# Kernel tuning notes

Measured on AMD Instinct MI355X. Metric: run time of the kernel, lower is better.

## Reference

```python
import jax, jax.numpy as jnp
import numpy as np

B, T, NG, NP, DV = 256, 100, 4096, 512, 2


def setup_inputs() -> dict:
    key = jax.random.key(0)
    k = jax.random.split(key, 6)
    v = jax.random.normal(k[0], (B, T, DV), dtype=jnp.float32) * 0.1
    P0 = jax.random.uniform(k[1], (B, NP), dtype=jnp.float32)
    # Dense kernels (glorot-ish scale); recurrent kernel uniform(-0.02, 0.02) per the module
    W_enc = jax.random.normal(k[2], (NP, NG), dtype=jnp.float32) / np.sqrt(NP)
    W_in = jax.random.normal(k[3], (DV, NG), dtype=jnp.float32) / np.sqrt(DV)
    W_rec = (jax.random.uniform(k[4], (NG, NG), dtype=jnp.float32) * 2.0 - 1.0) * 0.02
    W_dec = jax.random.normal(k[5], (NG, NP), dtype=jnp.float32) / np.sqrt(NG)
    return {"v": v, "P0": P0, "W_enc": W_enc, "W_in": W_in, "W_rec": W_rec, "W_dec": W_dec}


def reference(v, P0, W_enc, W_in, W_rec, W_dec):
    # encoder: init hidden state from place-cell code P0  -> [B, Ng]
    h0 = P0 @ W_enc
    # Precompute input projection for all timesteps: [B, T, Ng] -> scan over T
    xW = jnp.einsum('btd,dg->btg', v, W_in)
    xW_t = jnp.swapaxes(xW, 0, 1)  # [T, B, Ng]

    def step(h, x):
        h_new = jax.nn.relu(x + h @ W_rec)
        return h_new, h_new

    _, g = jax.lax.scan(step, h0, xW_t)      # g: [T, B, Ng]
    g = jnp.swapaxes(g, 0, 1)                # [B, T, Ng]
    place_preds = jnp.einsum('btg,gp->btp', g, W_dec)  # [B, T, Np]
    return place_preds
```

## Files before the change

kernel.cpp:

```cpp
#include <hip/hip_runtime.h>
#include <hip/hip_bf16.h>

typedef __attribute__((ext_vector_type(8))) short bf16x8;
typedef __attribute__((ext_vector_type(4))) float f32x4;

#define MFMA __builtin_amdgcn_mfma_f32_16x16x32_bf16

__device__ __forceinline__ short f2bf(float f) {
    union { __hip_bfloat16 h; short s; } u;
    u.h = __float2bfloat16(f);
    return u.s;
}

__global__ __launch_bounds__(64) void cvt_tile(const float* __restrict__ in,
                                               __hip_bfloat16* __restrict__ out, int C) {
    const int cd32 = C >> 5;
    const int tile = blockIdx.x;
    const int r16 = tile / cd32, c32 = tile - r16 * cd32;
    const int l = threadIdx.x;
    const int row = (r16 << 4) + (l & 15);
    const int c0 = (c32 << 5) + ((l >> 4) << 3);
    const float* src = in + (size_t)row * C + c0;
    short o[8];
#pragma unroll
    for (int j = 0; j < 8; ++j) o[j] = f2bf(src[j]);
    *(bf16x8*)((char*)out + (size_t)tile * 1024 + (l << 4)) = *(bf16x8*)o;
}

__global__ __launch_bounds__(256) void tcvt256(const float* __restrict__ in,
                                               __hip_bfloat16* __restrict__ out,
                                               int N, int K) {
    __shared__ float tile[64][65];
    const int r0 = blockIdx.x << 6;
    const int c0 = blockIdx.y << 6;
    const int tid = threadIdx.x;
    const int row = tid >> 2, cq = tid & 3;
#pragma unroll
    for (int it = 0; it < 4; ++it) {
        int c4 = cq + (it << 2);
        float4 vv = *(const float4*)(in + (size_t)(r0 + row) * N + c0 + (c4 << 2));
        tile[row][(c4 << 2) + 0] = vv.x;
        tile[row][(c4 << 2) + 1] = vv.y;
        tile[row][(c4 << 2) + 2] = vv.z;
        tile[row][(c4 << 2) + 3] = vv.w;
    }
    __syncthreads();
    const int kd32 = K >> 5;
#pragma unroll
    for (int half = 0; half < 2; ++half) {
        int slot = tid + (half << 8);
        int ti = slot >> 6, l = slot & 63;
        int ci = ti & 3, ri = ti >> 2;
        short o[8];
#pragma unroll
        for (int j = 0; j < 8; ++j)
            o[j] = f2bf(tile[(ri << 5) + ((l >> 4) << 3) + j][(ci << 4) + (l & 15)]);
        size_t tidx = (size_t)((c0 >> 4) + ci) * kd32 + (r0 >> 5) + ri;
        *(bf16x8*)((char*)out + tidx * 1024 + (l << 4)) = *(bf16x8*)o;
    }
}

template <int MODE, int NW, int KC>
__global__ __launch_bounds__(NW * 64) void gemm_r(const __hip_bfloat16* __restrict__ A,
                                                  const __hip_bfloat16* __restrict__ B,
                                                  void* __restrict__ outp,
                                                  const float* __restrict__ v,
                                                  const float* __restrict__ Wi, int t) {
    constexpr int KD32 = KC * NW;
    __shared__ __align__(16) char lds[NW * 16384];
    const int id = blockIdx.x;
    int bm, bn;
    if constexpr (MODE == 2) {
        int xcd = id & 7, idx = id >> 3;
        int sw = xcd * 400 + idx;
        bm = sw >> 3;
        bn = sw & 7;
    } else {
        int xcd = id & 7, j = id >> 3;
        bn = (xcd << 3) + (j & 7);
        bm = j >> 3;
    }
    const int tid = threadIdx.x, wv = tid >> 6, lane = tid & 63;
    char* myl = lds + (wv << 14);
    const int kw0 = wv * KC;
    const int bm4 = bm << 2, bn4 = bn << 2;

    constexpr size_t FSTR = (size_t)KD32 << 10;
    const char* pA = (const char*)A + (((size_t)(bm4 * KD32 + kw0)) << 10) + (lane << 4);
    const char* pB = (const char*)B + (((size_t)(bn4 * KD32 + kw0)) << 10) + (lane << 4);

    f32x4 acc[4][4] = {};
    bf16x8 A00, A01, A02, A03, A10, A11, A12, A13,
           A20, A21, A22, A23, A30, A31, A32, A33;
    bf16x8 B00, B01, B02, B03, B10, B11, B12, B13,
           B20, B21, B22, B23, B30, B31, B32, B33;

#define LOADG(S, KI)                                       \
    do {                                                   \
        const char* pa_ = pA + ((size_t)(KI) << 10);       \
        const char* pb_ = pB + ((size_t)(KI) << 10);       \
        A##S##0 = *(const bf16x8*)(pa_);                   \
        A##S##1 = *(const bf16x8*)(pa_ + FSTR);            \
        A##S##2 = *(const bf16x8*)(pa_ + 2 * FSTR);        \
        A##S##3 = *(const bf16x8*)(pa_ + 3 * FSTR);        \
        B##S##0 = *(const bf16x8*)(pb_);                   \
        B##S##1 = *(const bf16x8*)(pb_ + FSTR);            \
        B##S##2 = *(const bf16x8*)(pb_ + 2 * FSTR);        \
        B##S##3 = *(const bf16x8*)(pb_ + 3 * FSTR);        \
    } while (0)

#define COMPUTE(S)                                             \
    do {                                                       \
        acc[0][0] = MFMA(A##S##0, B##S##0, acc[0][0], 0, 0, 0);\
        acc[0][1] = MFMA(A##S##0, B##S##1, acc[0][1], 0, 0, 0);\
        acc[0][2] = MFMA(A##S##0, B##S##2, acc[0][2], 0, 0, 0);\
        acc[0][3] = MFMA(A##S##0, B##S##3, acc[0][3], 0, 0, 0);\
        acc[1][0] = MFMA(A##S##1, B##S##0, acc[1][0], 0, 0, 0);\
        acc[1][1] = MFMA(A##S##1, B##S##1, acc[1][1], 0, 0, 0);\
        acc[1][2] = MFMA(A##S##1, B##S##2, acc[1][2], 0, 0, 0);\
        acc[1][3] = MFMA(A##S##1, B##S##3, acc[1][3], 0, 0, 0);\
        acc[2][0] = MFMA(A##S##2, B##S##0, acc[2][0], 0, 0, 0);\
        acc[2][1] = MFMA(A##S##2, B##S##1, acc[2][1], 0, 0, 0);\
        acc[2][2] = MFMA(A##S##2, B##S##2, acc[2][2], 0, 0, 0);\
        acc[2][3] = MFMA(A##S##2, B##S##3, acc[2][3], 0, 0, 0);\
        acc[3][0] = MFMA(A##S##3, B##S##0, acc[3][0], 0, 0, 0);\
        acc[3][1] = MFMA(A##S##3, B##S##1, acc[3][1], 0, 0, 0);\
        acc[3][2] = MFMA(A##S##3, B##S##2, acc[3][2], 0, 0, 0);\
        acc[3][3] = MFMA(A##S##3, B##S##3, acc[3][3], 0, 0, 0);\
    } while (0)

#define ITER(S, SP, DOISS, KI)                  \
    do {                                        \
        if (DOISS) LOADG(SP, (KI) + 3);         \
        __builtin_amdgcn_sched_barrier(0);      \
        COMPUTE(S);                             \
        __builtin_amdgcn_sched_barrier(0);      \
    } while (0)

    LOADG(0, 0);
    __builtin_amdgcn_sched_barrier(0);
    LOADG(1, 1);
    __builtin_amdgcn_sched_barrier(0);
    LOADG(2, 2);
    __builtin_amdgcn_sched_barrier(0);

    int s = 0;
    for (; s + 4 < KC; s += 4) {
        ITER(0, 3, true, s + 0);
        ITER(1, 0, true, s + 1);
        ITER(2, 1, true, s + 2);
        ITER(3, 2, true, s + 3);
    }
    ITER(0, 3, true,  s + 0);
    ITER(1, 0, false, s + 1);
    ITER(2, 1, false, s + 2);
    ITER(3, 2, false, s + 3);

#undef ITER
#undef COMPUTE
#undef LOADG

#pragma unroll
    for (int f = 0; f < 4; ++f)
#pragma unroll
        for (int g = 0; g < 4; ++g)
            *(f32x4*)(myl + (((f << 2) + g) << 10) + (lane << 4)) = acc[f][g];
    __syncthreads();

    constexpr int FPW = 16 / NW;
    f32x4 fin[FPW];
#pragma unroll
    for (int q = 0; q < FPW; ++q) {
        const int fid = wv * FPW + q;
        f32x4 ssum = {};
#pragma unroll
        for (int w = 0; w < NW; ++w)
            ssum += *(const f32x4*)(lds + (w << 14) + (fid << 10) + (lane << 4));
        fin[q] = ssum;
    }

    if constexpr (MODE == 0 || MODE == 1) {
        char* O = (char*)outp;
#pragma unroll
        for (int q = 0; q < FPW; ++q) {
            const int fid = wv * FPW + q;
            const int fr = fid >> 2, g = fid & 3;
            const int rbase = (bm << 6) + (fr << 4) + ((lane >> 4) << 2);
            const int c = (bn << 6) + (g << 4) + (lane & 15);
#pragma unroll
            for (int j = 0; j < 4; ++j) {
                int r = rbase + j;
                float val = fin[q][j];
                if constexpr (MODE == 1) {
                    float v0 = v[(size_t)(r * 100 + t) * 2 + 0];
                    float v1 = v[(size_t)(r * 100 + t) * 2 + 1];
                    val = fmaxf(val + v0 * Wi[c] + v1 * Wi[4096 + c], 0.0f);
                }
                size_t off = ((size_t)(r >> 4) * 128 + (c >> 5)) * 1024 +
                             ((size_t)((r & 15) + (((c >> 3) & 3) << 4)) << 4) +
                             ((c & 7) << 1);
                *(short*)(O + off) = f2bf(val);
            }
        }
    } else {
        float* O = (float*)outp;
#pragma unroll
        for (int q = 0; q < FPW; ++q) {
            const int fid = wv * FPW + q;
            const int fr = fid >> 2, g = fid & 3;
            const int rbase = (bm << 6) + (fr << 4) + ((lane >> 4) << 2);
            const int c = (bn << 6) + (g << 4) + (lane & 15);
#pragma unroll
            for (int j = 0; j < 4; ++j) {
                int r = rbase + j;
                int tt = r >> 8;
                int b = r & 255;
                O[((size_t)b * 100 + tt) * 512 + c] = fin[q][j];
            }
        }
    }
}

extern "C" void kernel_launch(void* const* d_in, const int* in_sizes, int n_in,
                              void* d_out, int out_size, void* d_ws, size_t ws_size,
                              hipStream_t stream) {
    const float* v     = (const float*)d_in[0];
    const float* P0    = (const float*)d_in[1];
    const float* W_enc = (const float*)d_in[2];
    const float* W_in  = (const float*)d_in[3];
    const float* W_rec = (const float*)d_in[4];
    const float* W_dec = (const float*)d_in[5];
    float* out = (float*)d_out;

    char* ws = (char*)d_ws;
    __hip_bfloat16* Wrt = (__hip_bfloat16*)(ws + 0);
    __hip_bfloat16* Wet = (__hip_bfloat16*)(ws + 33554432);
    __hip_bfloat16* Wdt = (__hip_bfloat16*)(ws + 37748736);
    __hip_bfloat16* P0t = (__hip_bfloat16*)(ws + 41943040);
    __hip_bfloat16* h0  = (__hip_bfloat16*)(ws + 42205184);
    __hip_bfloat16* G   = (__hip_bfloat16*)(ws + 44302336);

    tcvt256<<<dim3(64, 64), 256, 0, stream>>>(W_rec, Wrt, 4096, 4096);
    tcvt256<<<dim3(8, 64), 256, 0, stream>>>(W_enc, Wet, 4096, 512);
    tcvt256<<<dim3(64, 8), 256, 0, stream>>>(W_dec, Wdt, 512, 4096);
    cvt_tile<<<256, 64, 0, stream>>>(P0, P0t, 512);

    gemm_r<0, 4, 4><<<256, 256, 0, stream>>>(P0t, Wet, (void*)h0, nullptr, nullptr, 0);

    for (int t = 0; t < 100; ++t) {
        const __hip_bfloat16* hprev = (t == 0) ? h0 : (G + (size_t)(t - 1) * 1048576);
        gemm_r<1, 4, 32><<<256, 256, 0, stream>>>(hprev, Wrt,
                                                  (void*)(G + (size_t)t * 1048576), v, W_in, t);
    }

    gemm_r<2, 4, 32><<<3200, 256, 0, stream>>>(G, Wdt, (void*)out, nullptr, nullptr, 0);
}
```

Measured before the change: 1.511 ms.

## Replace split-K decoder GEMM with dedicated 128x128 tiled kernel

The final decoder projection (25600x4096 by 4096x512) moves off the generic split-K gemm_r path, which used 64x64 tiles, 4 waves reducing over K through LDS, and 3200 blocks. It now uses a new gemm_d kernel with 128x128 output tiles, where each of the 4 waves owns a 64x64 sub-tile over the full K. This removes the LDS reduction and raises operand reuse per load, at the cost of longer per-wave K loops and only 800 blocks.

```diff
diff --git a/kernel.cpp b/kernel.cpp
--- a/kernel.cpp
+++ b/kernel.cpp
@@ -69,17 +69,9 @@
     constexpr int KD32 = KC * NW;
     __shared__ __align__(16) char lds[NW * 16384];
     const int id = blockIdx.x;
-    int bm, bn;
-    if constexpr (MODE == 2) {
-        int xcd = id & 7, idx = id >> 3;
-        int sw = xcd * 400 + idx;
-        bm = sw >> 3;
-        bn = sw & 7;
-    } else {
-        int xcd = id & 7, j = id >> 3;
-        bn = (xcd << 3) + (j & 7);
-        bm = j >> 3;
-    }
+    const int xcd = id & 7, j = id >> 3;
+    const int bn = (xcd << 3) + (j & 7);
+    const int bm = j >> 3;
     const int tid = threadIdx.x, wv = tid >> 6, lane = tid & 63;
     char* myl = lds + (wv << 14);
     const int kw0 = wv * KC;
@@ -179,43 +171,132 @@
         fin[q] = ssum;
     }
 
-    if constexpr (MODE == 0 || MODE == 1) {
-        char* O = (char*)outp;
-#pragma unroll
-        for (int q = 0; q < FPW; ++q) {
-            const int fid = wv * FPW + q;
-            const int fr = fid >> 2, g = fid & 3;
-            const int rbase = (bm << 6) + (fr << 4) + ((lane >> 4) << 2);
-            const int c = (bn << 6) + (g << 4) + (lane & 15);
-#pragma unroll
-            for (int j = 0; j < 4; ++j) {
-                int r = rbase + j;
-                float val = fin[q][j];
-                if constexpr (MODE == 1) {
-                    float v0 = v[(size_t)(r * 100 + t) * 2 + 0];
-                    float v1 = v[(size_t)(r * 100 + t) * 2 + 1];
-                    val = fmaxf(val + v0 * Wi[c] + v1 * Wi[4096 + c], 0.0f);
-                }
-                size_t off = ((size_t)(r >> 4) * 128 + (c >> 5)) * 1024 +
-                             ((size_t)((r & 15) + (((c >> 3) & 3) << 4)) << 4) +
-                             ((c & 7) << 1);
-                *(short*)(O + off) = f2bf(val);
+    char* O = (char*)outp;
+#pragma unroll
+    for (int q = 0; q < FPW; ++q) {
+        const int fid = wv * FPW + q;
+        const int fr = fid >> 2, g = fid & 3;
+        const int rbase = (bm << 6) + (fr << 4) + ((lane >> 4) << 2);
+        const int c = (bn << 6) + (g << 4) + (lane & 15);
+#pragma unroll
+        for (int j = 0; j < 4; ++j) {
+            int r = rbase + j;
+            float val = fin[q][j];
+            if constexpr (MODE == 1) {
+                float v0 = v[(size_t)(r * 100 + t) * 2 + 0];
+                float v1 = v[(size_t)(r * 100 + t) * 2 + 1];
+                val = fmaxf(val + v0 * Wi[c] + v1 * Wi[4096 + c], 0.0f);
             }
+            size_t off = ((size_t)(r >> 4) * 128 + (c >> 5)) * 1024 +
+                         ((size_t)((r & 15) + (((c >> 3) & 3) << 4)) << 4) +
+                         ((c & 7) << 1);
+            *(short*)(O + off) = f2bf(val);
         }
-    } else {
-        float* O = (float*)outp;
-#pragma unroll
-        for (int q = 0; q < FPW; ++q) {
-            const int fid = wv * FPW + q;
-            const int fr = fid >> 2, g = fid & 3;
-            const int rbase = (bm << 6) + (fr << 4) + ((lane >> 4) << 2);
-            const int c = (bn << 6) + (g << 4) + (lane & 15);
+    }
+}
+
+__global__ __launch_bounds__(256) void gemm_d(const __hip_bfloat16* __restrict__ G,
+                                              const __hip_bfloat16* __restrict__ Wdt,
+                                              float* __restrict__ out) {
+    constexpr int KD32 = 128;
+    const int id = blockIdx.x;
+    const int xcd = id & 7, idx = id >> 3;
+    const int sw = xcd * 100 + idx;
+    const int bm = sw >> 2;
+    const int bn = sw & 3;
+    const int tid = threadIdx.x, wv = tid >> 6, lane = tid & 63;
+    const int wr = wv >> 1, wc = wv & 1;
+
+    const int slab = bm >> 1, half = bm & 1;
+    constexpr size_t FSTR = (size_t)KD32 << 10;
+    const char* pA = (const char*)G + (size_t)slab * 2097152 +
+                     ((size_t)((half << 3) + (wr << 2)) << 17) + (lane << 4);
+    const char* pB = (const char*)Wdt +
+                     ((size_t)((bn << 3) + (wc << 2)) << 17) + (lane << 4);
+
+    f32x4 acc[4][4] = {};
+    bf16x8 A00, A01, A02, A03, A10, A11, A12, A13,
+           A20, A21, A22, A23, A30, A31, A32, A33;
+    bf16x8 B00, B01, B02, B03, B10, B11, B12, B13,
+           B20, B21, B22, B23, B30, B31, B32, B33;
+
+#define LOADG(S, KI)                                       \
+    do {                                                   \
+        const char* pa_ = pA + ((size_t)(KI) << 10);       \
+        const char* pb_ = pB + ((size_t)(KI) << 10);       \
+        A##S##0 = *(const bf16x8*)(pa_);                   \
+        A##S##1 = *(const bf16x8*)(pa_ + FSTR);            \
+        A##S##2 = *(const bf16x8*)(pa_ + 2 * FSTR);        \
+        A##S##3 = *(const bf16x8*)(pa_ + 3 * FSTR);        \
+        B##S##0 = *(const bf16x8*)(pb_);                   \
+        B##S##1 = *(const bf16x8*)(pb_ + FSTR);            \
+        B##S##2 = *(const bf16x8*)(pb_ + 2 * FSTR);        \
+        B##S##3 = *(const bf16x8*)(pb_ + 3 * FSTR);        \
+    } while (0)
+
+#define COMPUTE(S)                                             \
+    do {                                                       \
+        acc[0][0] = MFMA(A##S##0, B##S##0, acc[0][0], 0, 0, 0);\
+        acc[0][1] = MFMA(A##S##0, B##S##1, acc[0][1], 0, 0, 0);\
+        acc[0][2] = MFMA(A##S##0, B##S##2, acc[0][2], 0, 0, 0);\
+        acc[0][3] = MFMA(A##S##0, B##S##3, acc[0][3], 0, 0, 0);\
+        acc[1][0] = MFMA(A##S##1, B##S##0, acc[1][0], 0, 0, 0);\
+        acc[1][1] = MFMA(A##S##1, B##S##1, acc[1][1], 0, 0, 0);\
+        acc[1][2] = MFMA(A##S##1, B##S##2, acc[1][2], 0, 0, 0);\
+        acc[1][3] = MFMA(A##S##1, B##S##3, acc[1][3], 0, 0, 0);\
+        acc[2][0] = MFMA(A##S##2, B##S##0, acc[2][0], 0, 0, 0);\
+        acc[2][1] = MFMA(A##S##2, B##S##1, acc[2][1], 0, 0, 0);\
+        acc[2][2] = MFMA(A##S##2, B##S##2, acc[2][2], 0, 0, 0);\
+        acc[2][3] = MFMA(A##S##2, B##S##3, acc[2][3], 0, 0, 0);\
+        acc[3][0] = MFMA(A##S##3, B##S##0, acc[3][0], 0, 0, 0);\
+        acc[3][1] = MFMA(A##S##3, B##S##1, acc[3][1], 0, 0, 0);\
+        acc[3][2] = MFMA(A##S##3, B##S##2, acc[3][2], 0, 0, 0);\
+        acc[3][3] = MFMA(A##S##3, B##S##3, acc[3][3], 0, 0, 0);\
+    } while (0)
+
+#define ITER(S, SP, DOISS, KI)                  \
+    do {                                        \
+        if (DOISS) LOADG(SP, (KI) + 3);         \
+        __builtin_amdgcn_sched_barrier(0);      \
+        COMPUTE(S);                             \
+        __builtin_amdgcn_sched_barrier(0);      \
+    } while (0)
+
+    LOADG(0, 0);
+    __builtin_amdgcn_sched_barrier(0);
+    LOADG(1, 1);
+    __builtin_amdgcn_sched_barrier(0);
+    LOADG(2, 2);
+    __builtin_amdgcn_sched_barrier(0);
+
+    int s = 0;
+    for (; s + 4 < KD32; s += 4) {
+        ITER(0, 3, true, s + 0);
+        ITER(1, 0, true, s + 1);
+        ITER(2, 1, true, s + 2);
+        ITER(3, 2, true, s + 3);
+    }
+    ITER(0, 3, true,  s + 0);
+    ITER(1, 0, false, s + 1);
+    ITER(2, 1, false, s + 2);
+    ITER(3, 2, false, s + 3);
+
+#undef ITER
+#undef COMPUTE
+#undef LOADG
+
+#pragma unroll
+    for (int f = 0; f < 4; ++f) {
+        const int rbase = (bm << 7) + (wr << 6) + (f << 4) + ((lane >> 4) << 2);
+#pragma unroll
+        for (int g = 0; g < 4; ++g) {
+            const int c = (bn << 7) + (wc << 6) + (g << 4) + (lane & 15);
 #pragma unroll
             for (int j = 0; j < 4; ++j) {
                 int r = rbase + j;
                 int tt = r >> 8;
                 int b = r & 255;
-                O[((size_t)b * 100 + tt) * 512 + c] = fin[q][j];
+                out[((size_t)b * 100 + tt) * 512 + c] = acc[f][g][j];
             }
         }
     }
@@ -253,5 +334,5 @@
                                                   (void*)(G + (size_t)t * 1048576), v, W_in, t);
     }
 
-    gemm_r<2, 4, 32><<<3200, 256, 0, stream>>>(G, Wdt, (void*)out, nullptr, nullptr, 0);
-}
+    gemm_d<<<800, 256, 0, stream>>>(G, Wdt, out);
+}
```

New measurement: 1.525 ms. Within noise of the previous version (+0.9%).

## Replace decoder GEMM with dedicated LDS-staged kernel using direct global-to-LDS loads

Applied to the files above, without the earlier changes.

Adds a dedicated decoder kernel, gemm_dec, with 200 blocks of 512 threads. Each block computes a 256x256 output tile for one timestep over the full K=4096. W_dec tiles are staged into LDS with global_load_lds in a 4-slot pipeline shared by all waves, while each wave streams its own A rows straight into registers. This replaces the earlier 3200-block split-K kernel and its cross-wave LDS reduction, so shared B data is reused more and the reduction disappears. In exchange there are fewer blocks, so occupancy may be lower and the tail latency of each block is larger.

```diff
diff --git a/kernel.cpp b/kernel.cpp
--- a/kernel.cpp
+++ b/kernel.cpp
@@ -10,6 +10,12 @@
     union { __hip_bfloat16 h; short s; } u;
     u.h = __float2bfloat16(f);
     return u.s;
+}
+
+__device__ __forceinline__ void gld_lds16(const void* g, void* l) {
+    auto gp = (const __attribute__((address_space(1))) void*)(g);
+    auto lp = (__attribute__((address_space(3))) void*)(l);
+    __builtin_amdgcn_global_load_lds(gp, lp, 16, 0, 0);
 }
 
 __global__ __launch_bounds__(64) void cvt_tile(const float* __restrict__ in,
@@ -69,17 +75,9 @@
     constexpr int KD32 = KC * NW;
     __shared__ __align__(16) char lds[NW * 16384];
     const int id = blockIdx.x;
-    int bm, bn;
-    if constexpr (MODE == 2) {
-        int xcd = id & 7, idx = id >> 3;
-        int sw = xcd * 400 + idx;
-        bm = sw >> 3;
-        bn = sw & 7;
-    } else {
-        int xcd = id & 7, j = id >> 3;
-        bn = (xcd << 3) + (j & 7);
-        bm = j >> 3;
-    }
+    const int xcd = id & 7, j = id >> 3;
+    const int bn = (xcd << 3) + (j & 7);
+    const int bm = j >> 3;
     const int tid = threadIdx.x, wv = tid >> 6, lane = tid & 63;
     char* myl = lds + (wv << 14);
     const int kw0 = wv * KC;
@@ -179,44 +177,120 @@
         fin[q] = ssum;
     }
 
-    if constexpr (MODE == 0 || MODE == 1) {
-        char* O = (char*)outp;
-#pragma unroll
-        for (int q = 0; q < FPW; ++q) {
-            const int fid = wv * FPW + q;
-            const int fr = fid >> 2, g = fid & 3;
-            const int rbase = (bm << 6) + (fr << 4) + ((lane >> 4) << 2);
-            const int c = (bn << 6) + (g << 4) + (lane & 15);
-#pragma unroll
-            for (int j = 0; j < 4; ++j) {
-                int r = rbase + j;
-                float val = fin[q][j];
-                if constexpr (MODE == 1) {
-                    float v0 = v[(size_t)(r * 100 + t) * 2 + 0];
-                    float v1 = v[(size_t)(r * 100 + t) * 2 + 1];
-                    val = fmaxf(val + v0 * Wi[c] + v1 * Wi[4096 + c], 0.0f);
-                }
-                size_t off = ((size_t)(r >> 4) * 128 + (c >> 5)) * 1024 +
-                             ((size_t)((r & 15) + (((c >> 3) & 3) << 4)) << 4) +
-                             ((c & 7) << 1);
-                *(short*)(O + off) = f2bf(val);
+    char* O = (char*)outp;
+#pragma unroll
+    for (int q = 0; q < FPW; ++q) {
+        const int fid = wv * FPW + q;
+        const int fr = fid >> 2, g = fid & 3;
+        const int rbase = (bm << 6) + (fr << 4) + ((lane >> 4) << 2);
+        const int c = (bn << 6) + (g << 4) + (lane & 15);
+#pragma unroll
+        for (int j = 0; j < 4; ++j) {
+            int r = rbase + j;
+            float val = fin[q][j];
+            if constexpr (MODE == 1) {
+                float v0 = v[(size_t)(r * 100 + t) * 2 + 0];
+                float v1 = v[(size_t)(r * 100 + t) * 2 + 1];
+                val = fmaxf(val + v0 * Wi[c] + v1 * Wi[4096 + c], 0.0f);
             }
+            size_t off = ((size_t)(r >> 4) * 128 + (c >> 5)) * 1024 +
+                         ((size_t)((r & 15) + (((c >> 3) & 3) << 4)) << 4) +
+                         ((c & 7) << 1);
+            *(short*)(O + off) = f2bf(val);
         }
-    } else {
-        float* O = (float*)outp;
-#pragma unroll
-        for (int q = 0; q < FPW; ++q) {
-            const int fid = wv * FPW + q;
-            const int fr = fid >> 2, g = fid & 3;
-            const int rbase = (bm << 6) + (fr << 4) + ((lane >> 4) << 2);
-            const int c = (bn << 6) + (g << 4) + (lane & 15);
-#pragma unroll
-            for (int j = 0; j < 4; ++j) {
-                int r = rbase + j;
-                int tt = r >> 8;
-                int b = r & 255;
-                O[((size_t)b * 100 + tt) * 512 + c] = fin[q][j];
-            }
+    }
+}
+
+__global__ __launch_bounds__(512) void gemm_dec(const __hip_bfloat16* __restrict__ G,
+                                                const __hip_bfloat16* __restrict__ Wdt,
+                                                float* __restrict__ out) {
+    __shared__ __align__(16) char lds[65536];
+    const int id = blockIdx.x;
+    const int t = id >> 1, nh = id & 1;
+    const int tid = threadIdx.x, wv = tid >> 6, lane = tid & 63;
+
+    const char* pA = (const char*)G + (size_t)t * 2097152 +
+                     ((size_t)(wv << 1) << 17) + (lane << 4);
+    const char* pB = (const char*)Wdt + ((size_t)(nh << 4) << 17) + (lane << 4);
+
+    f32x4 acc0[16] = {};
+    f32x4 acc1[16] = {};
+    bf16x8 A00, A01, A10, A11, A20, A21, A30, A31;
+
+#define STAGE(SLOT, KI)                                                  \
+    do {                                                                 \
+        char* d_ = lds + ((SLOT) << 14);                                 \
+        const char* b_ = pB + (((size_t)(wv << 1)) << 17) +              \
+                         ((size_t)(KI) << 10);                           \
+        gld_lds16(b_, d_ + ((wv << 1) << 10));                           \
+        gld_lds16(b_ + (1 << 17), d_ + (((wv << 1) + 1) << 10));         \
+    } while (0)
+
+#define LOADA(S, KI)                                                     \
+    do {                                                                 \
+        const char* a_ = pA + ((size_t)(KI) << 10);                      \
+        A##S##0 = *(const bf16x8*)(a_);                                  \
+        A##S##1 = *(const bf16x8*)(a_ + (1 << 17));                      \
+    } while (0)
+
+#define COMPUTE(S)                                                       \
+    do {                                                                 \
+        const char* bb_ = lds + ((S) << 14) + (lane << 4);               \
+        _Pragma("unroll") for (int f = 0; f < 16; ++f) {                 \
+            bf16x8 b_ = *(const bf16x8*)(bb_ + (f << 10));               \
+            acc0[f] = MFMA(A##S##0, b_, acc0[f], 0, 0, 0);               \
+            acc1[f] = MFMA(A##S##1, b_, acc1[f], 0, 0, 0);               \
+        }                                                                \
+    } while (0)
+
+#define ITER(S, SP, VM, DOISS, KI)                                 \
+    do {                                                           \
+        asm volatile("s_waitcnt vmcnt(%0)" ::"i"(VM) : "memory");  \
+        __builtin_amdgcn_s_barrier();                              \
+        __builtin_amdgcn_sched_barrier(0);                         \
+        if (DOISS) {                                               \
+            STAGE(SP, (KI) + 3);                                   \
+            LOADA(SP, (KI) + 3);                                   \
+        }                                                          \
+        __builtin_amdgcn_sched_barrier(0);                         \
+        COMPUTE(S);                                                \
+    } while (0)
+
+    STAGE(0, 0); LOADA(0, 0);
+    __builtin_amdgcn_sched_barrier(0);
+    STAGE(1, 1); LOADA(1, 1);
+    __builtin_amdgcn_sched_barrier(0);
+    STAGE(2, 2); LOADA(2, 2);
+    __builtin_amdgcn_sched_barrier(0);
+
+    int s = 0;
+    for (; s + 4 < 128; s += 4) {
+        ITER(0, 3, 8, true, s + 0);
+        ITER(1, 0, 8, true, s + 1);
+        ITER(2, 1, 8, true, s + 2);
+        ITER(3, 2, 8, true, s + 3);
+    }
+    ITER(0, 3, 8, true,  s + 0);
+    ITER(1, 0, 8, false, s + 1);
+    ITER(2, 1, 4, false, s + 2);
+    ITER(3, 2, 0, false, s + 3);
+
+#undef ITER
+#undef COMPUTE
+#undef LOADA
+#undef STAGE
+
+    const int rb = (wv << 5) + ((lane >> 4) << 2);
+    const int cb = (nh << 8) + (lane & 15);
+#pragma unroll
+    for (int f = 0; f < 16; ++f) {
+        const int c = cb + (f << 4);
+#pragma unroll
+        for (int j = 0; j < 4; ++j) {
+            int b0 = rb + j;
+            int b1 = rb + 16 + j;
+            out[((size_t)b0 * 100 + t) * 512 + c] = acc0[f][j];
+            out[((size_t)b1 * 100 + t) * 512 + c] = acc1[f][j];
         }
     }
 }
@@ -253,5 +327,5 @@
                                                   (void*)(G + (size_t)t * 1048576), v, W_in, t);
     }
 
-    gemm_r<2, 4, 32><<<3200, 256, 0, stream>>>(G, Wdt, (void*)out, nullptr, nullptr, 0);
-}
+    gemm_dec<<<200, 512, 0, stream>>>(G, Wdt, out);
+}
```

After: 1.468 ms (median of 2 runs). 2.9% less time.
